# Optimization experiments

Hardware: AMD Instinct MI355X
Metric: run time of the kernel (lower is better)

## Reference

```python
import jax, jax.numpy as jnp
import numpy as np

B, T, D = 4, 2048, 1024
H, Dh = 16, 64
Q_LAT, KV_LAT, O_LAT = 512, 256, 512
ROPE = 32
FFN_RANK, FFN_INTER = 384, 4096
EPS = 1e-6
THETA = 10000.0


def rms_norm(x, w, eps=EPS):
    xf = x.astype(jnp.float32)
    var = jnp.mean(xf * xf, axis=-1, keepdims=True)
    return (w * (xf * jax.lax.rsqrt(var + eps))).astype(x.dtype)


def rotate_half(x):
    x1, x2 = jnp.split(x, 2, axis=-1)
    return jnp.concatenate([-x2, x1], axis=-1)


def setup_inputs() -> dict:
    key = jax.random.key(0)
    ks = jax.random.split(key, 12)
    s = lambda fan_in: 1.0 / np.sqrt(fan_in)
    inp = {
        "hidden_states": jax.random.normal(ks[0], (B, T, D), jnp.float32),
        "ln1_w": jnp.ones((D,), jnp.float32),
        "a_ln_w": jnp.ones((Q_LAT + KV_LAT,), jnp.float32),
        "qkv_a_w": jax.random.normal(ks[1], (D, Q_LAT + KV_LAT), jnp.float32) * s(D),
        "q_b_w": jax.random.normal(ks[2], (Q_LAT, H * Dh), jnp.float32) * s(Q_LAT),
        "kv_b_w": jax.random.normal(ks[3], (KV_LAT, 2 * H * Dh), jnp.float32) * s(KV_LAT),
        "o_a_w": jax.random.normal(ks[4], (H * Dh, O_LAT), jnp.float32) * s(H * Dh),
        "o_b_w": jax.random.normal(ks[5], (O_LAT, D), jnp.float32) * s(O_LAT),
        "ln2_w": jnp.ones((D,), jnp.float32),
        "ffn_in_a": jax.random.normal(ks[6], (D, FFN_RANK), jnp.float32) * s(D),
        "ffn_in_b": jax.random.normal(ks[7], (FFN_RANK, FFN_INTER), jnp.float32) * s(FFN_RANK),
        "ffn_out_a": jax.random.normal(ks[8], (FFN_INTER, FFN_RANK), jnp.float32) * s(FFN_INTER),
        "ffn_out_b": jax.random.normal(ks[9], (FFN_RANK, D), jnp.float32) * s(FFN_RANK),
    }
    # RoPE tables over first ROPE dims of each head
    inv_freq = 1.0 / (THETA ** (np.arange(0, ROPE, 2, dtype=np.float32) / ROPE))
    t = np.arange(T, dtype=np.float32)
    freqs = np.outer(t, inv_freq)                      # [T, ROPE/2]
    emb = np.concatenate([freqs, freqs], axis=-1)      # [T, ROPE]
    inp["cos"] = jnp.asarray(np.cos(emb), jnp.float32)
    inp["sin"] = jnp.asarray(np.sin(emb), jnp.float32)
    return inp


def reference(hidden_states, cos, sin, ln1_w, a_ln_w, qkv_a_w, q_b_w, kv_b_w,
              o_a_w, o_b_w, ln2_w, ffn_in_a, ffn_in_b, ffn_out_a, ffn_out_b):
    x = hidden_states
    # --- MLA attention (pre-norm) ---
    h = rms_norm(x, ln1_w)
    lat = rms_norm(h @ qkv_a_w, a_ln_w)                # [B,T,Q_LAT+KV_LAT]
    q_lat, kv_lat = jnp.split(lat, [Q_LAT], axis=-1)
    q = (q_lat @ q_b_w).reshape(B, T, H, Dh).transpose(0, 2, 1, 3)   # [B,H,T,Dh]
    kv = (kv_lat @ kv_b_w).reshape(B, T, H, 2 * Dh).transpose(0, 2, 1, 3)
    k, v = jnp.split(kv, 2, axis=-1)
    # partial RoPE on first ROPE dims
    c = cos[None, None]; s_ = sin[None, None]          # [1,1,T,ROPE]
    q_r, q_p = q[..., :ROPE], q[..., ROPE:]
    k_r, k_p = k[..., :ROPE], k[..., ROPE:]
    q = jnp.concatenate([q_r * c + rotate_half(q_r) * s_, q_p], axis=-1)
    k = jnp.concatenate([k_r * c + rotate_half(k_r) * s_, k_p], axis=-1)
    scores = jnp.einsum("bhqd,bhkd->bhqk", q, k) * (Dh ** -0.5)
    attn = jax.nn.softmax(scores, axis=-1)
    ctx = jnp.einsum("bhqk,bhkd->bhqd", attn, v)
    ctx = ctx.transpose(0, 2, 1, 3).reshape(B, T, H * Dh)
    attn_out = (ctx @ o_a_w) @ o_b_w                   # output subspace
    x = x + attn_out
    # --- decomposed FFN (pre-norm) ---
    h2 = rms_norm(x, ln2_w)
    ff = jax.nn.gelu((h2 @ ffn_in_a) @ ffn_in_b)
    ff = (ff @ ffn_out_a) @ ffn_out_b
    return x + ff
```

## Files before the change

### kernel.cpp

```cpp
#include <hip/hip_runtime.h>
#include <hip/hip_bf16.h>
#include <stdint.h>

#define NTOK 8192

typedef unsigned short u16;
typedef __attribute__((ext_vector_type(4))) float f32x4;
typedef __attribute__((ext_vector_type(8))) short s16x8;
typedef __attribute__((ext_vector_type(4))) short s16x4;
typedef __attribute__((ext_vector_type(8))) u16   u16x8;
typedef __attribute__((ext_vector_type(4))) u16   u16x4;
typedef __attribute__((ext_vector_type(4))) uint32_t u32x4;

__device__ __forceinline__ float fast_exp2(float x) {
    return __builtin_amdgcn_exp2f(x);
}
__device__ __forceinline__ u16 f2bf(float f) {
    uint32_t u = __float_as_uint(f);
    u = (u + 0x7FFFu + ((u >> 16) & 1u)) >> 16;
    return (u16)u;
}
__device__ __forceinline__ float bf2f(u16 h) {
    return __uint_as_float(((uint32_t)h) << 16);
}
__device__ __forceinline__ void async_cp16(const void* g, void* l) {
    __builtin_amdgcn_global_load_lds(
        (const __attribute__((address_space(1))) void*)g,
        (__attribute__((address_space(3))) void*)l, 16, 0, 0);
}
__device__ __forceinline__ void wait_vm4()   { asm volatile("s_waitcnt vmcnt(4)" ::: "memory"); }
__device__ __forceinline__ void wait_vm0()   { asm volatile("s_waitcnt vmcnt(0)" ::: "memory"); }
__device__ __forceinline__ void wait_lgkm0() { asm volatile("s_waitcnt lgkmcnt(0)" ::: "memory"); }
__device__ __forceinline__ void raw_barrier(){ asm volatile("s_barrier" ::: "memory"); }

__device__ __forceinline__ void xcd_tile(int& bx, int& by) {
    int gx = gridDim.x;
    int nwg = gx * gridDim.y;
    int flat = blockIdx.y * gx + blockIdx.x;
    int swz = (flat & 7) * (nwg >> 3) + (flat >> 3);
    bx = swz % gx;
    by = swz / gx;
}

struct TDesc { const float* s; u16* d; int K; int N; int tile0; };
struct TPack { TDesc t[8]; };

__global__ __launch_bounds__(256) void k_transpose_all(TPack p)
{
    __shared__ float tile[32][33];
    int bid = blockIdx.x;
    int i = 0;
    #pragma unroll
    for (int j = 1; j < 8; j++) if (bid >= p.t[j].tile0) i = j;
    const float* src = p.t[i].s;
    u16* dst = p.t[i].d;
    int K = p.t[i].K, N = p.t[i].N;
    int local = bid - p.t[i].tile0;
    int nx = N >> 5;
    int n0 = (local % nx) * 32, k0 = (local / nx) * 32;
    int tx = threadIdx.x, ty = threadIdx.y;
    #pragma unroll
    for (int r = 0; r < 32; r += 8)
        tile[ty + r][tx] = src[(size_t)(k0 + ty + r) * N + n0 + tx];
    __syncthreads();
    #pragma unroll
    for (int r = 0; r < 32; r += 8)
        dst[(size_t)(n0 + ty + r) * K + k0 + tx] = f2bf(tile[tx][ty + r]);
}

__global__ __launch_bounds__(256) void k_cvt(
    const float* __restrict__ in, u16* __restrict__ out)
{
    int i = (blockIdx.x * 256 + threadIdx.x) * 4;
    f32x4 v = *(const f32x4*)&in[i];
    u16x4 o;
    #pragma unroll
    for (int j = 0; j < 4; j++) o[j] = f2bf(v[j]);
    *(u16x4*)&out[i] = o;
}

template<int W>
__global__ __launch_bounds__(256) void k_rmsnorm(
    const float* __restrict__ x, const float* __restrict__ w, u16* __restrict__ out)
{
    constexpr int E = W / 256;
    int row = blockIdx.x, tid = threadIdx.x;
    const float* xr = x + (size_t)row * W;
    float v[E]; float ss = 0.f;
    #pragma unroll
    for (int i = 0; i < E; i++) { v[i] = xr[tid + i * 256]; ss += v[i] * v[i]; }
    #pragma unroll
    for (int m = 1; m < 64; m <<= 1) ss += __shfl_xor(ss, m, 64);
    __shared__ float red[4];
    if ((tid & 63) == 0) red[tid >> 6] = ss;
    __syncthreads();
    ss = red[0] + red[1] + red[2] + red[3];
    float scale = rsqrtf(ss / (float)W + 1e-6f);
    u16* orow = out + (size_t)row * W;
    #pragma unroll
    for (int i = 0; i < E; i++)
        orow[tid + i * 256] = f2bf(w[tid + i * 256] * (v[i] * scale));
}

template<int EPI>
__global__ __launch_bounds__(256) void k_gemm(
    const u16* __restrict__ A, int lda,
    const u16* __restrict__ Bt, int ldb,
    int M, int N, int K,
    float* __restrict__ outF, u16* __restrict__ outB,
    const float* __restrict__ resid)
{
    __shared__ __align__(16) u16 As[2][4096];
    __shared__ __align__(16) u16 Bs[2][4096];
    int tid = threadIdx.x;
    int w = tid >> 6, lane = tid & 63;
    int bx, by; xcd_tile(bx, by);
    int m0 = by * 128, n0 = bx * 128;
    int wm = w & 1, wn = w >> 1;
    int lr = lane & 15, lq = lane >> 4;

    f32x4 acc[4][4];
    #pragma unroll
    for (int i = 0; i < 4; i++)
        #pragma unroll
        for (int j = 0; j < 4; j++) acc[i][j] = (f32x4)(0.f);

    int ar = tid >> 2;
    int ac = (tid & 3) * 8;
    const u16* Ag = A  + (size_t)(m0 + ar) * lda + ac;
    const u16* Bg = Bt + (size_t)(n0 + ar) * ldb + ac;
    int lo = w * 512;

    auto stage = [&](int kt, int s) {
        const u16* a  = Ag + kt * 32;
        const u16* bp = Bg + kt * 32;
        async_cp16(a,                     &As[s][lo]);
        async_cp16(a + (size_t)64 * lda,  &As[s][lo + 2048]);
        async_cp16(bp,                    &Bs[s][lo]);
        async_cp16(bp + (size_t)64 * ldb, &Bs[s][lo + 2048]);
    };

    int nk = K >> 5;
    stage(0, 0);
    stage(1, 1);
    for (int k = 0; k < nk; k++) {
        if (k + 1 < nk) wait_vm4(); else wait_vm0();
        raw_barrier();
        int s = k & 1;
        s16x8 af[4], bfr[4];
        #pragma unroll
        for (int ms = 0; ms < 4; ms++)
            af[ms] = *reinterpret_cast<const s16x8*>(&As[s][(wm * 64 + ms * 16 + lr) * 32 + lq * 8]);
        #pragma unroll
        for (int ns = 0; ns < 4; ns++)
            bfr[ns] = *reinterpret_cast<const s16x8*>(&Bs[s][(wn * 64 + ns * 16 + lr) * 32 + lq * 8]);
        #pragma unroll
        for (int ms = 0; ms < 4; ms++)
            #pragma unroll
            for (int ns = 0; ns < 4; ns++)
                acc[ms][ns] = __builtin_amdgcn_mfma_f32_16x16x32_bf16(af[ms], bfr[ns], acc[ms][ns], 0, 0, 0);
        wait_lgkm0();
        raw_barrier();
        if (k + 2 < nk) stage(k + 2, s);
    }

    #pragma unroll
    for (int ms = 0; ms < 4; ms++) {
        #pragma unroll
        for (int ns = 0; ns < 4; ns++) {
            int col = n0 + wn * 64 + ns * 16 + lr;
            #pragma unroll
            for (int r = 0; r < 4; r++) {
                int row = m0 + wm * 64 + ms * 16 + lq * 4 + r;
                float v = acc[ms][ns][r];
                size_t idx = (size_t)row * N + col;
                if (EPI == 0) {
                    outF[idx] = v;
                } else if (EPI == 1) {
                    outB[idx] = f2bf(v);
                } else if (EPI == 2) {
                    float t = 0.7978845608028654f * (v + 0.044715f * v * v * v);
                    float e = fast_exp2(t * 2.8853900817779268f);
                    outB[idx] = f2bf(v - v * __builtin_amdgcn_rcpf(1.f + e));
                } else {
                    outF[idx] = v + resid[idx];
                }
            }
        }
    }
}

template<int EPI>
__global__ __launch_bounds__(256) void k_gemm64(
    const u16* __restrict__ A, int lda,
    const u16* __restrict__ Bt, int ldb,
    int M, int N, int K,
    float* __restrict__ outF, u16* __restrict__ outB)
{
    __shared__ __align__(16) u16 As[2][4096];
    __shared__ __align__(16) u16 Bs[2][4096];
    int tid = threadIdx.x;
    int w = tid >> 6, lane = tid & 63;
    int bx, by; xcd_tile(bx, by);
    int m0 = by * 64, n0 = bx * 64;
    int wm = w & 1, wn = w >> 1;
    int lr = lane & 15, lq = lane >> 4;

    f32x4 acc[2][2];
    #pragma unroll
    for (int i = 0; i < 2; i++)
        #pragma unroll
        for (int j = 0; j < 2; j++) acc[i][j] = (f32x4)(0.f);

    int srow = tid >> 2;
    int sq   = tid & 3;
    const u16* Ag = A  + (size_t)(m0 + srow) * lda + sq * 8;
    const u16* Bg = Bt + (size_t)(n0 + srow) * ldb + sq * 8;
    int lo = srow * 32 + sq * 8;

    auto stage = [&](int kt, int s) {
        const u16* a  = Ag + kt * 64;
        const u16* bp = Bg + kt * 64;
        async_cp16(a,       &As[s][lo]);
        async_cp16(a + 32,  &As[s][2048 + lo]);
        async_cp16(bp,      &Bs[s][lo]);
        async_cp16(bp + 32, &Bs[s][2048 + lo]);
    };

    int nk = K >> 6;
    stage(0, 0);
    stage(1, 1);
    for (int k = 0; k < nk; k++) {
        if (k + 1 < nk) wait_vm4(); else wait_vm0();
        raw_barrier();
        int s = k & 1;
        s16x8 af[2][2], bfr[2][2];
        #pragma unroll
        for (int kc = 0; kc < 2; kc++) {
            #pragma unroll
            for (int ms = 0; ms < 2; ms++)
                af[ms][kc] = *reinterpret_cast<const s16x8*>(
                    &As[s][kc * 2048 + (wm * 32 + ms * 16 + lr) * 32 + lq * 8]);
            #pragma unroll
            for (int ns = 0; ns < 2; ns++)
                bfr[ns][kc] = *reinterpret_cast<const s16x8*>(
                    &Bs[s][kc * 2048 + (wn * 32 + ns * 16 + lr) * 32 + lq * 8]);
        }
        #pragma unroll
        for (int kc = 0; kc < 2; kc++)
            #pragma unroll
            for (int ms = 0; ms < 2; ms++)
                #pragma unroll
                for (int ns = 0; ns < 2; ns++)
                    acc[ms][ns] = __builtin_amdgcn_mfma_f32_16x16x32_bf16(
                        af[ms][kc], bfr[ns][kc], acc[ms][ns], 0, 0, 0);
        wait_lgkm0();
        raw_barrier();
        if (k + 2 < nk) stage(k + 2, s);
    }

    #pragma unroll
    for (int ms = 0; ms < 2; ms++) {
        #pragma unroll
        for (int ns = 0; ns < 2; ns++) {
            int col = n0 + wn * 32 + ns * 16 + lr;
            #pragma unroll
            for (int r = 0; r < 4; r++) {
                int row = m0 + wm * 32 + ms * 16 + lq * 4 + r;
                float v = acc[ms][ns][r];
                size_t idx = (size_t)row * N + col;
                if (EPI == 0) outF[idx] = v;
                else          outB[idx] = f2bf(v);
            }
        }
    }
}

__global__ __launch_bounds__(256) void k_rope(
    const u16* __restrict__ q, const u16* __restrict__ kv,
    const float* __restrict__ cosb, const float* __restrict__ sinb,
    u16* __restrict__ q_r, u16* __restrict__ k_r)
{
    const float QS = 0.125f * 1.4426950408889634f;
    int idx = blockIdx.x * 256 + threadIdx.x;
    int g = idx & 7;
    int h = (idx >> 3) & 15;
    int t = (idx >> 7) & 2047;
    int b = idx >> 18;
    size_t qsrc = ((size_t)((b * 2048 + t) * 16 + h)) * 64 + g * 8;
    size_t ksrc = ((size_t)((b * 2048 + t) * 16 + h)) * 128 + g * 8;
    u16x8 qa = *(const u16x8*)&q[qsrc];
    u16x8 ka = *(const u16x8*)&kv[ksrc];
    u16x8 qo, ko;
    if (g < 4) {
        int pd = ((g ^ 2) - g) * 8;
        u16x8 qp = *(const u16x8*)&q[qsrc + pd];
        u16x8 kp = *(const u16x8*)&kv[ksrc + pd];
        float sgn = (g < 2) ? -1.f : 1.f;
        const float* cp = &cosb[t * 32 + g * 8];
        const float* sp = &sinb[t * 32 + g * 8];
        #pragma unroll
        for (int j = 0; j < 8; j++) {
            float c = cp[j], s = sp[j];
            qo[j] = f2bf((bf2f(qa[j]) * c + sgn * bf2f(qp[j]) * s) * QS);
            ko[j] = f2bf(bf2f(ka[j]) * c + sgn * bf2f(kp[j]) * s);
        }
    } else {
        #pragma unroll
        for (int j = 0; j < 8; j++) {
            qo[j] = f2bf(bf2f(qa[j]) * QS);
            ko[j] = ka[j];
        }
    }
    size_t dst = ((size_t)(b * 16 + h) * 2048 + t) * 64 + g * 8;
    *(u16x8*)&q_r[dst] = qo;
    *(u16x8*)&k_r[dst] = ko;
}

__global__ __launch_bounds__(256) void k_vtrans(
    const u16* __restrict__ kv, u16* __restrict__ v_t)
{
    __shared__ u16 tile[64][72];
    int bh = blockIdx.y;
    int b = bh >> 4, h = bh & 15;
    int t0 = blockIdx.x * 64;
    int tid = threadIdx.x;
    int r = tid >> 2;
    int c4 = (tid & 3) * 16;
    const u16* src = kv + ((size_t)((b * 2048 + t0 + r) * 16 + h)) * 128 + 64;
    #pragma unroll
    for (int j = 0; j < 16; j += 8)
        *(u16x8*)&tile[r][c4 + j] = *(const u16x8*)&src[c4 + j];
    __syncthreads();
    int dd = tid >> 2;
    u16* dst = v_t + ((size_t)bh * 64 + dd) * 2048 + t0;
    #pragma unroll
    for (int j0 = 0; j0 < 16; j0 += 8) {
        u16x8 vv;
        #pragma unroll
        for (int j = 0; j < 8; j++) vv[j] = tile[c4 + j0 + j][dd];
        *(u16x8*)&dst[c4 + j0] = vv;
    }
}

__global__ __launch_bounds__(256) void k_attn(
    const u16* __restrict__ q_r, const u16* __restrict__ k_r,
    const u16* __restrict__ v_t, u16* __restrict__ ctx)
{
    __shared__ __align__(16) u16 Ks[2][4096];
    __shared__ __align__(16) u16 Vs[2][4096];
    int tid = threadIdx.x, w = tid >> 6, lane = tid & 63;
    int flat = blockIdx.x;
    int xcd = flat & 7;
    int idx = flat >> 3;
    int bh  = xcd * 8 + (idx & 7);
    int xb  = idx >> 3;
    int b = bh >> 4, h = bh & 15;
    int q0 = xb * 128 + w * 32;
    const u16* Qp = q_r + (size_t)bh * 2048 * 64;
    const u16* Kp = k_r + (size_t)bh * 2048 * 64;
    const u16* Vp = v_t + (size_t)bh * 64 * 2048;
    int lr = lane & 15, lq = lane >> 4;
    int swz = (lr >> 1) & 3;

    s16x8 qf[2][2];
    #pragma unroll
    for (int qc = 0; qc < 2; qc++)
        #pragma unroll
        for (int kf = 0; kf < 2; kf++)
            qf[qc][kf] = *(const s16x8*)&Qp[(size_t)(q0 + qc * 16 + lr) * 64 + kf * 32 + lq * 8];

    s16x8 ones;
    #pragma unroll
    for (int j = 0; j < 8; j++) ones[j] = (short)0x3F80;

    f32x4 fz = (f32x4)(0.f);
    asm("" : "+v"(fz));

    int schunk = ((lane & 3) ^ ((lane >> 3) & 3)) * 8;
    const u16* gp;
    u16 *lp0, *lp1;
    size_t grow;
    int gAdv;
    if (w < 2) {
        gp = Kp + (size_t)(lane >> 2) * 64 + w * 32 + schunk;
        lp0 = &Ks[0][w * 2048]; lp1 = &Ks[1][w * 2048];
        grow = 16 * 64;  gAdv = 64 * 64;
    } else {
        gp = Vp + (size_t)(lane >> 2) * 2048 + (w - 2) * 32 + schunk;
        lp0 = &Vs[0][(w - 2) * 2048]; lp1 = &Vs[1][(w - 2) * 2048];
        grow = 16 * 2048; gAdv = 64;
    }
    auto stageP = [&](u16* lp) {
        #pragma unroll
        for (int g = 0; g < 4; g++)
            async_cp16(gp + g * grow, lp + g * 512);
        gp += gAdv;
    };

    f32x4 o[2][4];
    #pragma unroll
    for (int qt = 0; qt < 2; qt++)
        #pragma unroll
        for (int ds = 0; ds < 4; ds++) o[qt][ds] = (f32x4)(0.f);
    f32x4 lacc0 = (f32x4)(0.f), lacc1 = (f32x4)(0.f);

#define ATTN_BODY(S)                                                           \
  {                                                                            \
    f32x4 sc[2][4];                                                            \
    __builtin_amdgcn_s_setprio(1);                                             \
    _Pragma("unroll")                                                          \
    for (int ns = 0; ns < 4; ns++) {                                           \
      int ko = (ns * 16 + lr) * 32 + ((lq ^ swz) * 8);                         \
      s16x8 a0 = *(const s16x8*)&Ks[S][ko];                                    \
      s16x8 a1 = *(const s16x8*)&Ks[S][2048 + ko];                             \
      _Pragma("unroll")                                                        \
      for (int qc = 0; qc < 2; qc++) {                                         \
        f32x4 t;                                                               \
        t = __builtin_amdgcn_mfma_f32_16x16x32_bf16(a0, qf[qc][0], fz, 0, 0, 0);\
        t = __builtin_amdgcn_mfma_f32_16x16x32_bf16(a1, qf[qc][1], t, 0, 0, 0);\
        sc[qc][ns] = t;                                                        \
      }                                                                        \
    }                                                                          \
    __builtin_amdgcn_s_setprio(0);                                             \
    _Pragma("unroll")                                                          \
    for (int kf = 0; kf < 2; kf++) {                                           \
      u32x4 w0, w1;                                                            \
      _Pragma("unroll")                                                        \
      for (int j = 0; j < 4; j++) {                                            \
        int ns = kf * 2 + (j >> 1);                                            \
        int r0 = (j & 1) * 2;                                                  \
        float ea = fast_exp2(sc[0][ns][r0]);                                   \
        float eb = fast_exp2(sc[0][ns][r0 + 1]);                               \
        float ec = fast_exp2(sc[1][ns][r0]);                                   \
        float ed = fast_exp2(sc[1][ns][r0 + 1]);                               \
        uint32_t t0, t1;                                                       \
        asm("v_cvt_pk_bf16_f32 %0, %1, %2" : "=v"(t0) : "v"(ea), "v"(eb));     \
        asm("v_cvt_pk_bf16_f32 %0, %1, %2" : "=v"(t1) : "v"(ec), "v"(ed));     \
        w0[j] = t0; w1[j] = t1;                                                \
      }                                                                        \
      s16x8 pk0 = __builtin_bit_cast(s16x8, w0);                               \
      s16x8 pk1 = __builtin_bit_cast(s16x8, w1);                               \
      __builtin_amdgcn_s_setprio(1);                                           \
      lacc0 = __builtin_amdgcn_mfma_f32_16x16x32_bf16(pk0, ones, lacc0, 0,0,0);\
      lacc1 = __builtin_amdgcn_mfma_f32_16x16x32_bf16(pk1, ones, lacc1, 0,0,0);\
      _Pragma("unroll")                                                        \
      for (int ds = 0; ds < 4; ds++) {                                         \
        int vbase = kf * 2048 + (ds * 16 + lr) * 32 + (lq & 1) * 4;            \
        s16x4 vlo = *(const s16x4*)&Vs[S][vbase + (((lq >> 1)    ) ^ swz) * 8];\
        s16x4 vhi = *(const s16x4*)&Vs[S][vbase + (((lq >> 1) | 2) ^ swz) * 8];\
        s16x8 vf = __builtin_shufflevector(vlo, vhi, 0, 1, 2, 3, 4, 5, 6, 7);  \
        o[0][ds] = __builtin_amdgcn_mfma_f32_16x16x32_bf16(pk0, vf, o[0][ds], 0, 0, 0);\
        o[1][ds] = __builtin_amdgcn_mfma_f32_16x16x32_bf16(pk1, vf, o[1][ds], 0, 0, 0);\
      }                                                                        \
      __builtin_amdgcn_s_setprio(0);                                           \
    }                                                                          \
  }

    stageP(lp0);
    stageP(lp1);
    for (int k2 = 0; k2 < 15; k2++) {
        wait_vm4(); raw_barrier();
        ATTN_BODY(0)
        wait_lgkm0(); raw_barrier();
        stageP(lp0);
        wait_vm4(); raw_barrier();
        ATTN_BODY(1)
        wait_lgkm0(); raw_barrier();
        stageP(lp1);
    }
    wait_vm4(); raw_barrier();
    ATTN_BODY(0)
    wait_vm0(); raw_barrier();
    ATTN_BODY(1)
#undef ATTN_BODY

    #pragma unroll
    for (int qt = 0; qt < 2; qt++) {
        f32x4 lv = qt ? lacc1 : lacc0;
        float li[4];
        #pragma unroll
        for (int r = 0; r < 4; r++) li[r] = __builtin_amdgcn_rcpf(lv[r]);
        #pragma unroll
        for (int ds = 0; ds < 4; ds++)
            #pragma unroll
            for (int r = 0; r < 4; r++) {
                int tq = q0 + qt * 16 + lq * 4 + r;
                float v = o[qt][ds][r] * li[r];
                ctx[((size_t)(b * 2048) + tq) * 1024 + h * 64 + ds * 16 + lr] = f2bf(v);
            }
    }
}

extern "C" void kernel_launch(void* const* d_in, const int* in_sizes, int n_in,
                              void* d_out, int out_size, void* d_ws, size_t ws_size,
                              hipStream_t stream) {
    (void)in_sizes; (void)n_in; (void)out_size; (void)ws_size;
    const float* x     = (const float*)d_in[0];
    const float* ln1   = (const float*)d_in[1];
    const float* alnw  = (const float*)d_in[2];
    const float* qkv_a = (const float*)d_in[3];
    const float* q_b   = (const float*)d_in[4];
    const float* kv_b  = (const float*)d_in[5];
    const float* o_a   = (const float*)d_in[6];
    const float* o_b   = (const float*)d_in[7];
    const float* ln2   = (const float*)d_in[8];
    const float* in_a  = (const float*)d_in[9];
    const float* in_b  = (const float*)d_in[10];
    const float* out_a = (const float*)d_in[11];
    const float* out_b = (const float*)d_in[12];
    const float* cosb  = (const float*)d_in[13];
    const float* sinb  = (const float*)d_in[14];
    float* out = (float*)d_out;
    char* ws = (char*)d_ws;

    u16* wqkv = (u16*)ws;
    u16* wq   = wqkv + 786432;
    u16* wkv  = wq   + 524288;
    u16* wob  = wkv  + 524288;
    u16* wia  = wob  + 524288;
    u16* wib  = wia  + 393216;
    u16* woa2 = wib  + 1572864;
    u16* wob2 = woa2 + 1572864;
    u16* woan = wob2 + 393216;
    u16* woab = woan + 524288;

    char* G = ws + 15728640;
    u16*  hbuf  = (u16*)(G + 0);
    float* lat_raw = (float*)(G + 16777216);
    u16*  lat   = (u16*)(G + 41943040);
    u16*  qbuf  = (u16*)(G + 54525952);
    u16*  kvbuf = (u16*)(G + 71303168);
    u16*  q_r   = (u16*)(G + 0);
    u16*  k_r   = (u16*)(G + 16777216);
    u16*  v_t   = (u16*)(G + 33554432);
    u16*  ctx   = (u16*)(G + 54525952);
    float* x2   = (float*)(G + 0);
    u16*  h2    = (u16*)(G + 33554432);
    u16*  t1    = (u16*)(G + 50331648);
    u16*  t2    = (u16*)(G + 56623104);
    u16*  t3    = (u16*)(G + 50331648);

    TPack tp;
    tp.t[0] = { qkv_a, wqkv, 1024, 768,  0 };
    tp.t[1] = { q_b,   wq,   512,  1024, 768 };
    tp.t[2] = { kv_b,  wkv,  256,  2048, 1280 };
    tp.t[3] = { o_b,   wob,  512,  1024, 1792 };
    tp.t[4] = { in_a,  wia,  1024, 384,  2304 };
    tp.t[5] = { in_b,  wib,  384,  4096, 2688 };
    tp.t[6] = { out_a, woa2, 4096, 384,  4224 };
    tp.t[7] = { out_b, wob2, 384,  1024, 5760 };
    k_transpose_all<<<6144, dim3(32, 8), 0, stream>>>(tp);
    k_cvt<<<512, 256, 0, stream>>>(o_a, woan);
    k_gemm64<1><<<dim3(16, 16), 256, 0, stream>>>(wob, 512, woan, 512, 1024, 1024, 512, nullptr, woab);

    k_rmsnorm<1024><<<NTOK, 256, 0, stream>>>(x, ln1, hbuf);
    k_gemm64<0><<<dim3(12, 128), 256, 0, stream>>>(hbuf, 1024, wqkv, 1024, NTOK, 768, 1024, lat_raw, nullptr);
    k_rmsnorm<768><<<NTOK, 256, 0, stream>>>(lat_raw, alnw, lat);
    k_gemm<1><<<dim3(8, 64),  256, 0, stream>>>(lat,       768, wq,  512, NTOK, 1024, 512, nullptr, qbuf,  nullptr);
    k_gemm<1><<<dim3(16, 64), 256, 0, stream>>>(lat + 512, 768, wkv, 256, NTOK, 2048, 256, nullptr, kvbuf, nullptr);
    k_rope<<<4096, 256, 0, stream>>>(qbuf, kvbuf, cosb, sinb, q_r, k_r);
    k_vtrans<<<dim3(32, 64), 256, 0, stream>>>(kvbuf, v_t);
    k_attn<<<1024, 256, 0, stream>>>(q_r, k_r, v_t, ctx);
    k_gemm<3><<<dim3(8, 64), 256, 0, stream>>>(ctx, 1024, woab, 1024, NTOK, 1024, 1024, x2, nullptr, x);
    k_rmsnorm<1024><<<NTOK, 256, 0, stream>>>(x2, ln2, h2);
    k_gemm64<1><<<dim3(6, 128), 256, 0, stream>>>(h2, 1024, wia, 1024, NTOK, 384, 1024, nullptr, t1);
    k_gemm<2><<<dim3(32, 64), 256, 0, stream>>>(t1, 384, wib, 384, NTOK, 4096, 384, nullptr, t2, nullptr);
    k_gemm64<1><<<dim3(6, 128), 256, 0, stream>>>(t2, 4096, woa2, 4096, NTOK, 384, 4096, nullptr, t3);
    k_gemm<3><<<dim3(8, 64), 256, 0, stream>>>(t3, 384, wob2, 384, NTOK, 1024, 384, out, nullptr, x2);
}
```

Baseline: 466.3 us.

## Fuse RoPE, Q scaling and V transpose into Q/KV projection GEMM epilogues

```diff
diff --git a/kernel.cpp b/kernel.cpp
--- a/kernel.cpp
+++ b/kernel.cpp
@@ -108,7 +108,9 @@
     const u16* __restrict__ Bt, int ldb,
     int M, int N, int K,
     float* __restrict__ outF, u16* __restrict__ outB,
-    const float* __restrict__ resid)
+    const float* __restrict__ resid,
+    const float* __restrict__ cosP, const float* __restrict__ sinP,
+    u16* __restrict__ outB2)
 {
     __shared__ __align__(16) u16 As[2][4096];
     __shared__ __align__(16) u16 Bs[2][4096];
@@ -164,27 +166,95 @@
         if (k + 2 < nk) stage(k + 2, s);
     }
 
-    #pragma unroll
-    for (int ms = 0; ms < 4; ms++) {
-        #pragma unroll
-        for (int ns = 0; ns < 4; ns++) {
-            int col = n0 + wn * 64 + ns * 16 + lr;
+    if constexpr (EPI <= 3) {
+        #pragma unroll
+        for (int ms = 0; ms < 4; ms++) {
+            #pragma unroll
+            for (int ns = 0; ns < 4; ns++) {
+                int col = n0 + wn * 64 + ns * 16 + lr;
+                #pragma unroll
+                for (int r = 0; r < 4; r++) {
+                    int row = m0 + wm * 64 + ms * 16 + lq * 4 + r;
+                    float v = acc[ms][ns][r];
+                    size_t idx = (size_t)row * N + col;
+                    if (EPI == 0) {
+                        outF[idx] = v;
+                    } else if (EPI == 1) {
+                        outB[idx] = f2bf(v);
+                    } else if (EPI == 2) {
+                        float t = 0.7978845608028654f * (v + 0.044715f * v * v * v);
+                        float e = fast_exp2(t * 2.8853900817779268f);
+                        outB[idx] = f2bf(v - v * __builtin_amdgcn_rcpf(1.f + e));
+                    } else {
+                        outF[idx] = v + resid[idx];
+                    }
+                }
+            }
+        }
+    } else if constexpr (EPI == 4) {
+        const float QS = 0.125f * 1.4426950408889634f;
+        int h = (n0 >> 6) + wn;
+        #pragma unroll
+        for (int ms = 0; ms < 4; ms++) {
             #pragma unroll
             for (int r = 0; r < 4; r++) {
                 int row = m0 + wm * 64 + ms * 16 + lq * 4 + r;
-                float v = acc[ms][ns][r];
-                size_t idx = (size_t)row * N + col;
-                if (EPI == 0) {
-                    outF[idx] = v;
-                } else if (EPI == 1) {
-                    outB[idx] = f2bf(v);
-                } else if (EPI == 2) {
-                    float t = 0.7978845608028654f * (v + 0.044715f * v * v * v);
-                    float e = fast_exp2(t * 2.8853900817779268f);
-                    outB[idx] = f2bf(v - v * __builtin_amdgcn_rcpf(1.f + e));
-                } else {
-                    outF[idx] = v + resid[idx];
+                int b = row >> 11, t = row & 2047;
+                u16* dst = outB + ((size_t)(b * 16 + h) * 2048 + t) * 64;
+                float x0 = acc[ms][0][r], x1 = acc[ms][1][r];
+                float c0 = cosP[t * 32 + lr],      s0 = sinP[t * 32 + lr];
+                float c1 = cosP[t * 32 + 16 + lr], s1 = sinP[t * 32 + 16 + lr];
+                dst[lr]      = f2bf((x0 * c0 - x1 * s0) * QS);
+                dst[16 + lr] = f2bf((x1 * c1 + x0 * s1) * QS);
+                dst[32 + lr] = f2bf(acc[ms][2][r] * QS);
+                dst[48 + lr] = f2bf(acc[ms][3][r] * QS);
+            }
+        }
+    } else {
+        int h  = n0 >> 7;
+        int b  = m0 >> 11;
+        int t0 = m0 & 2047;
+        if (wn == 0) {
+            #pragma unroll
+            for (int ms = 0; ms < 4; ms++) {
+                #pragma unroll
+                for (int r = 0; r < 4; r++) {
+                    int row = m0 + wm * 64 + ms * 16 + lq * 4 + r;
+                    int t = row & 2047;
+                    u16* dst = outB + ((size_t)(b * 16 + h) * 2048 + t) * 64;
+                    float x0 = acc[ms][0][r], x1 = acc[ms][1][r];
+                    float c0 = cosP[t * 32 + lr],      s0 = sinP[t * 32 + lr];
+                    float c1 = cosP[t * 32 + 16 + lr], s1 = sinP[t * 32 + 16 + lr];
+                    dst[lr]      = f2bf(x0 * c0 - x1 * s0);
+                    dst[16 + lr] = f2bf(x1 * c1 + x0 * s1);
+                    dst[32 + lr] = f2bf(acc[ms][2][r]);
+                    dst[48 + lr] = f2bf(acc[ms][3][r]);
                 }
+            }
+        } else {
+            u16* vb = wm ? (u16*)Bs : (u16*)As;
+            #pragma unroll
+            for (int ms = 0; ms < 4; ms++)
+                #pragma unroll
+                for (int ns = 0; ns < 4; ns++)
+                    #pragma unroll
+                    for (int r = 0; r < 4; r++)
+                        vb[(ms * 16 + lq * 4 + r) * 68 + ns * 16 + lr] =
+                            f2bf(acc[ms][ns][r]);
+        }
+        raw_barrier();
+        if (wn == 1) {
+            int idxv = (w - 2) * 64 + lane;
+            int dv = idxv >> 1;
+            int th = (idxv & 1) * 64;
+            const u16* rb = th ? (const u16*)Bs : (const u16*)As;
+            u16* dst = outB2 + ((size_t)(b * 16 + h) * 64 + dv) * 2048 + t0 + th;
+            #pragma unroll
+            for (int j0 = 0; j0 < 64; j0 += 8) {
+                u16x8 vv;
+                #pragma unroll
+                for (int j = 0; j < 8; j++) vv[j] = rb[(j0 + j) * 68 + dv];
+                *(u16x8*)&dst[j0] = vv;
             }
         }
     }
@@ -273,73 +343,6 @@
                 else          outB[idx] = f2bf(v);
             }
         }
-    }
-}
-
-__global__ __launch_bounds__(256) void k_rope(
-    const u16* __restrict__ q, const u16* __restrict__ kv,
-    const float* __restrict__ cosb, const float* __restrict__ sinb,
-    u16* __restrict__ q_r, u16* __restrict__ k_r)
-{
-    const float QS = 0.125f * 1.4426950408889634f;
-    int idx = blockIdx.x * 256 + threadIdx.x;
-    int g = idx & 7;
-    int h = (idx >> 3) & 15;
-    int t = (idx >> 7) & 2047;
-    int b = idx >> 18;
-    size_t qsrc = ((size_t)((b * 2048 + t) * 16 + h)) * 64 + g * 8;
-    size_t ksrc = ((size_t)((b * 2048 + t) * 16 + h)) * 128 + g * 8;
-    u16x8 qa = *(const u16x8*)&q[qsrc];
-    u16x8 ka = *(const u16x8*)&kv[ksrc];
-    u16x8 qo, ko;
-    if (g < 4) {
-        int pd = ((g ^ 2) - g) * 8;
-        u16x8 qp = *(const u16x8*)&q[qsrc + pd];
-        u16x8 kp = *(const u16x8*)&kv[ksrc + pd];
-        float sgn = (g < 2) ? -1.f : 1.f;
-        const float* cp = &cosb[t * 32 + g * 8];
-        const float* sp = &sinb[t * 32 + g * 8];
-        #pragma unroll
-        for (int j = 0; j < 8; j++) {
-            float c = cp[j], s = sp[j];
-            qo[j] = f2bf((bf2f(qa[j]) * c + sgn * bf2f(qp[j]) * s) * QS);
-            ko[j] = f2bf(bf2f(ka[j]) * c + sgn * bf2f(kp[j]) * s);
-        }
-    } else {
-        #pragma unroll
-        for (int j = 0; j < 8; j++) {
-            qo[j] = f2bf(bf2f(qa[j]) * QS);
-            ko[j] = ka[j];
-        }
-    }
-    size_t dst = ((size_t)(b * 16 + h) * 2048 + t) * 64 + g * 8;
-    *(u16x8*)&q_r[dst] = qo;
-    *(u16x8*)&k_r[dst] = ko;
-}
-
-__global__ __launch_bounds__(256) void k_vtrans(
-    const u16* __restrict__ kv, u16* __restrict__ v_t)
-{
-    __shared__ u16 tile[64][72];
-    int bh = blockIdx.y;
-    int b = bh >> 4, h = bh & 15;
-    int t0 = blockIdx.x * 64;
-    int tid = threadIdx.x;
-    int r = tid >> 2;
-    int c4 = (tid & 3) * 16;
-    const u16* src = kv + ((size_t)((b * 2048 + t0 + r) * 16 + h)) * 128 + 64;
-    #pragma unroll
-    for (int j = 0; j < 16; j += 8)
-        *(u16x8*)&tile[r][c4 + j] = *(const u16x8*)&src[c4 + j];
-    __syncthreads();
-    int dd = tid >> 2;
-    u16* dst = v_t + ((size_t)bh * 64 + dd) * 2048 + t0;
-    #pragma unroll
-    for (int j0 = 0; j0 < 16; j0 += 8) {
-        u16x8 vv;
-        #pragma unroll
-        for (int j = 0; j < 8; j++) vv[j] = tile[c4 + j0 + j][dd];
-        *(u16x8*)&dst[c4 + j0] = vv;
     }
 }
 
@@ -529,11 +532,9 @@
     u16*  hbuf  = (u16*)(G + 0);
     float* lat_raw = (float*)(G + 16777216);
     u16*  lat   = (u16*)(G + 41943040);
-    u16*  qbuf  = (u16*)(G + 54525952);
-    u16*  kvbuf = (u16*)(G + 71303168);
     u16*  q_r   = (u16*)(G + 0);
     u16*  k_r   = (u16*)(G + 16777216);
-    u16*  v_t   = (u16*)(G + 33554432);
+    u16*  v_t   = (u16*)(G + 71303168);
     u16*  ctx   = (u16*)(G + 54525952);
     float* x2   = (float*)(G + 0);
     u16*  h2    = (u16*)(G + 33554432);
@@ -557,15 +558,18 @@
     k_rmsnorm<1024><<<NTOK, 256, 0, stream>>>(x, ln1, hbuf);
     k_gemm64<0><<<dim3(12, 128), 256, 0, stream>>>(hbuf, 1024, wqkv, 1024, NTOK, 768, 1024, lat_raw, nullptr);
     k_rmsnorm<768><<<NTOK, 256, 0, stream>>>(lat_raw, alnw, lat);
-    k_gemm<1><<<dim3(8, 64),  256, 0, stream>>>(lat,       768, wq,  512, NTOK, 1024, 512, nullptr, qbuf,  nullptr);
-    k_gemm<1><<<dim3(16, 64), 256, 0, stream>>>(lat + 512, 768, wkv, 256, NTOK, 2048, 256, nullptr, kvbuf, nullptr);
-    k_rope<<<4096, 256, 0, stream>>>(qbuf, kvbuf, cosb, sinb, q_r, k_r);
-    k_vtrans<<<dim3(32, 64), 256, 0, stream>>>(kvbuf, v_t);
+    k_gemm<4><<<dim3(8, 64),  256, 0, stream>>>(lat,       768, wq,  512, NTOK, 1024, 512,
+                                                nullptr, q_r, nullptr, cosb, sinb, nullptr);
+    k_gemm<5><<<dim3(16, 64), 256, 0, stream>>>(lat + 512, 768, wkv, 256, NTOK, 2048, 256,
+                                                nullptr, k_r, nullptr, cosb, sinb, v_t);
     k_attn<<<1024, 256, 0, stream>>>(q_r, k_r, v_t, ctx);
-    k_gemm<3><<<dim3(8, 64), 256, 0, stream>>>(ctx, 1024, woab, 1024, NTOK, 1024, 1024, x2, nullptr, x);
+    k_gemm<3><<<dim3(8, 64), 256, 0, stream>>>(ctx, 1024, woab, 1024, NTOK, 1024, 1024,
+                                               x2, nullptr, x, nullptr, nullptr, nullptr);
     k_rmsnorm<1024><<<NTOK, 256, 0, stream>>>(x2, ln2, h2);
     k_gemm64<1><<<dim3(6, 128), 256, 0, stream>>>(h2, 1024, wia, 1024, NTOK, 384, 1024, nullptr, t1);
-    k_gemm<2><<<dim3(32, 64), 256, 0, stream>>>(t1, 384, wib, 384, NTOK, 4096, 384, nullptr, t2, nullptr);
+    k_gemm<2><<<dim3(32, 64), 256, 0, stream>>>(t1, 384, wib, 384, NTOK, 4096, 384,
+                                                nullptr, t2, nullptr, nullptr, nullptr, nullptr);
     k_gemm64<1><<<dim3(6, 128), 256, 0, stream>>>(t2, 4096, woa2, 4096, NTOK, 384, 4096, nullptr, t3);
-    k_gemm<3><<<dim3(8, 64), 256, 0, stream>>>(t3, 384, wob2, 384, NTOK, 1024, 384, out, nullptr, x2);
-}
+    k_gemm<3><<<dim3(8, 64), 256, 0, stream>>>(t3, 384, wob2, 384, NTOK, 1024, 384,
+                                               out, nullptr, x2, nullptr, nullptr, nullptr);
+}
```

Result: faster. 451.5 us (-3.2%).
